# Optimization experiments

Measured on AMD Instinct MI355X. Metric: run time of the kernel, lower is better.

The kernel has to match this reference:

```python
import jax, jax.numpy as jnp
import numpy as np

B, P, ENC_DIM = 256, 196, 2048
WORD_DIM, ATT_DIM = 512, 512

def setup_inputs() -> dict:
    key = jax.random.key(0)
    ks = jax.random.split(key, 8)
    s_enc = 1.0 / np.sqrt(ENC_DIM)
    s_dec = 1.0 / np.sqrt(WORD_DIM)
    s_fin = 1.0 / np.sqrt(ATT_DIM)
    return {
        "encoder_out": jax.random.normal(ks[0], (B, P, ENC_DIM), dtype=jnp.float32),
        "decoder_out": jax.random.normal(ks[1], (B, WORD_DIM), dtype=jnp.float32),
        "W_enc": jax.random.uniform(ks[2], (ENC_DIM, ATT_DIM), jnp.float32, -s_enc, s_enc),
        "b_enc": jax.random.uniform(ks[3], (ATT_DIM,), jnp.float32, -s_enc, s_enc),
        "W_dec": jax.random.uniform(ks[4], (WORD_DIM, ATT_DIM), jnp.float32, -s_dec, s_dec),
        "b_dec": jax.random.uniform(ks[5], (ATT_DIM,), jnp.float32, -s_dec, s_dec),
        "W_fin": jax.random.uniform(ks[6], (ATT_DIM,), jnp.float32, -s_fin, s_fin),
        "b_fin": jax.random.uniform(ks[7], (), jnp.float32, -s_fin, s_fin),
    }

def reference(encoder_out, decoder_out, W_enc, b_enc, W_dec, b_dec, W_fin, b_fin):
    # encoder projection: [B, P, A]
    att_enc = jnp.einsum('bpe,ea->bpa', encoder_out, W_enc) + b_enc
    # decoder projection: [B, A]
    att_dec = decoder_out @ W_dec + b_dec
    # additive combine + relu + final scalar projection -> [B, P]
    hidden = jax.nn.relu(att_enc + att_dec[:, None, :])
    att = jnp.einsum('bpa,a->bp', hidden, W_fin) + b_fin
    # softmax over pixels (dim=1)
    att_weights = jax.nn.softmax(att, axis=1)
    # weighted sum of encoder features -> [B, ENC_DIM]
    return jnp.einsum('bpe,bp->be', encoder_out, att_weights)
```

## Files before the change

### kernel.cpp

```cpp
#include <hip/hip_runtime.h>

#define B_   256
#define P_   196
#define E_   2048
#define WD_  512
#define A_   512
#define M_   (B_ * P_)

typedef __bf16 bf16x8 __attribute__((ext_vector_type(8)));
typedef float  f32x4  __attribute__((ext_vector_type(4)));

using u16 = unsigned short;
using u32 = unsigned int;

__device__ inline u16 f2bf(float f) {
    u32 u; __builtin_memcpy(&u, &f, 4);
    u += 0x7FFFu + ((u >> 16) & 1u); return (u16)(u >> 16);
}

__global__ __launch_bounds__(256) void k_prep(const float* __restrict__ We,
                                              u16* __restrict__ Wt) {
    __shared__ float tile[32][33];
    const int tx = threadIdx.x & 31, ty = threadIdx.x >> 5;
    const int k0 = blockIdx.x * 32, n0 = blockIdx.y * 32;
#pragma unroll
    for (int i = 0; i < 4; ++i)
        tile[ty + i * 8][tx] = We[(size_t)(k0 + ty + i * 8) * A_ + n0 + tx];
    __syncthreads();
#pragma unroll
    for (int i = 0; i < 4; ++i)
        Wt[(size_t)(n0 + ty + i * 8) * E_ + k0 + tx] = f2bf(tile[tx][ty + i * 8]);
}

__global__ __launch_bounds__(512) void k_att_dec(const float* __restrict__ dec,
                                                 const float* __restrict__ Wd,
                                                 const float* __restrict__ bd,
                                                 float* __restrict__ att_dec) {
    int b = blockIdx.x, a = threadIdx.x;
    __shared__ float sd[WD_];
    sd[a] = dec[b * WD_ + a];
    __syncthreads();
    float acc = bd[a];
#pragma unroll 8
    for (int e = 0; e < WD_; ++e)
        acc = fmaf(sd[e], Wd[e * A_ + a], acc);
    att_dec[b * A_ + a] = acc;
}

__global__ __launch_bounds__(512, 2) void k_logits(
        const float* __restrict__ enc, const u16* __restrict__ Wt,
        const float* __restrict__ be, const float* __restrict__ Wf,
        const float* __restrict__ att_dec, float* __restrict__ att) {
    __shared__ bf16x8 sA[2][256];
    __shared__ float  sred[8][64];

    const int t   = threadIdx.x;
    const int w   = t >> 6;
    const int L   = t & 63;
    const int l15 = L & 15;
    const int q   = L >> 4;
    const int m0  = blockIdx.x * 64;

    const f32x4 zero = {0.f, 0.f, 0.f, 0.f};
    f32x4 acc[4][4];
#pragma unroll
    for (int rt = 0; rt < 4; ++rt)
#pragma unroll
        for (int ct = 0; ct < 4; ++ct) acc[rt][ct] = zero;

    const int s    = t >> 1, h = t & 1;
    const int srt  = s >> 6;
    const int sL   = s & 63;
    const float* ap = enc + (size_t)(m0 + srt * 16 + (sL & 15)) * E_
                          + (sL >> 4) * 8 + h * 4;
    u32* slds = (u32*)&sA[0][s] + h * 2;
    u32* slds1 = (u32*)&sA[1][s] + h * 2;

    const u16* bp = Wt + (size_t)(w * 64 + l15) * E_ + q * 8;
    const size_t bstep = (size_t)16 * E_;

    uint4 bcur[4], bnxt[4];
#pragma unroll
    for (int ct = 0; ct < 4; ++ct)
        bcur[ct] = *(const uint4*)(bp + ct * bstep);
    float4 aN1 = *(const float4*)(ap);
    float4 aN2 = *(const float4*)(ap + 32);
    {
        u32 lo = (u32)f2bf(aN1.x) | ((u32)f2bf(aN1.y) << 16);
        u32 hi = (u32)f2bf(aN1.z) | ((u32)f2bf(aN1.w) << 16);
        slds[0] = lo; slds[1] = hi;
    }
    aN1 = aN2;
    __syncthreads();

    for (int k = 0; k < 64; ++k) {
        const int buf = k & 1;
        bf16x8 af[4];
#pragma unroll
        for (int rt = 0; rt < 4; ++rt) af[rt] = sA[buf][rt * 64 + L];

        const int kA = (k + 2 < 64) ? k + 2 : 63;
        const int kB = (k + 1 < 64) ? k + 1 : 63;
        aN2 = *(const float4*)(ap + (size_t)kA * 32);
#pragma unroll
        for (int ct = 0; ct < 4; ++ct)
            bnxt[ct] = *(const uint4*)(bp + ct * bstep + (size_t)kB * 32);

#pragma unroll
        for (int ct = 0; ct < 4; ++ct) {
            bf16x8 bv; __builtin_memcpy(&bv, &bcur[ct], 16);
#pragma unroll
            for (int rt = 0; rt < 4; ++rt)
                acc[rt][ct] = __builtin_amdgcn_mfma_f32_16x16x32_bf16(
                    af[rt], bv, acc[rt][ct], 0, 0, 0);
        }

        {
            u32 lo = (u32)f2bf(aN1.x) | ((u32)f2bf(aN1.y) << 16);
            u32 hi = (u32)f2bf(aN1.z) | ((u32)f2bf(aN1.w) << 16);
            u32* d = buf ? slds : slds1;
            d[0] = lo; d[1] = hi;
        }
        aN1 = aN2;
#pragma unroll
        for (int ct = 0; ct < 4; ++ct) bcur[ct] = bnxt[ct];
        __syncthreads();
    }

    float wf[4], bev[4];
#pragma unroll
    for (int ct = 0; ct < 4; ++ct) {
        int n = w * 64 + ct * 16 + l15;
        wf[ct]  = Wf[n];
        bev[ct] = be[n];
    }
#pragma unroll
    for (int rt = 0; rt < 4; ++rt) {
#pragma unroll
        for (int reg = 0; reg < 4; ++reg) {
            int ml = rt * 16 + q * 4 + reg;
            int b  = (m0 + ml) / P_;
            const float* adp = att_dec + (size_t)b * A_ + w * 64 + l15;
            float p = 0.f;
#pragma unroll
            for (int ct = 0; ct < 4; ++ct) {
                float hx = acc[rt][ct][reg] + bev[ct] + adp[ct * 16];
                p = fmaf(fmaxf(hx, 0.f), wf[ct], p);
            }
#pragma unroll
            for (int off = 8; off > 0; off >>= 1)
                p += __shfl_down(p, off, 16);
            if (l15 == 0) sred[w][ml] = p;
        }
    }
    __syncthreads();
    if (t < 64) {
        float r = 0.f;
#pragma unroll
        for (int ww = 0; ww < 8; ++ww) r += sred[ww][t];
        att[m0 + t] = r;
    }
}

__global__ __launch_bounds__(256) void k_out(const float* __restrict__ enc,
                                             const float* __restrict__ att,
                                             float* __restrict__ out) {
    int b = blockIdx.x, t = threadIdx.x;
    __shared__ float sw[P_];
    __shared__ float red[8];
    __shared__ f32x4 spart[4][64];

    float v = (t < P_) ? att[b * P_ + t] : -1e30f;
    float m = v;
#pragma unroll
    for (int off = 32; off > 0; off >>= 1)
        m = fmaxf(m, __shfl_down(m, off, 64));
    int wid = t >> 6;
    if ((t & 63) == 0) red[wid] = m;
    __syncthreads();
    m = fmaxf(fmaxf(red[0], red[1]), fmaxf(red[2], red[3]));

    float ev = (t < P_) ? __expf(v - m) : 0.f;
    float ssum = ev;
#pragma unroll
    for (int off = 32; off > 0; off >>= 1)
        ssum += __shfl_down(ssum, off, 64);
    if ((t & 63) == 0) red[4 + wid] = ssum;
    __syncthreads();
    ssum = red[4] + red[5] + red[6] + red[7];
    if (t < P_) sw[t] = ev / ssum;
    __syncthreads();

    const int tq = t >> 6, lane = t & 63;
    const int e0 = blockIdx.y * 256 + lane * 4;
    const float* ep = enc + (size_t)b * P_ * E_ + e0;
    f32x4 acc = {0.f, 0.f, 0.f, 0.f};
    const int p0 = tq * 49;
#pragma unroll 7
    for (int i = 0; i < 49; ++i) {
        int p = p0 + i;
        float4 qv = *(const float4*)(ep + (size_t)p * E_);
        float wgt = sw[p];
        acc[0] = fmaf(wgt, qv.x, acc[0]);
        acc[1] = fmaf(wgt, qv.y, acc[1]);
        acc[2] = fmaf(wgt, qv.z, acc[2]);
        acc[3] = fmaf(wgt, qv.w, acc[3]);
    }
    spart[tq][lane] = acc;
    __syncthreads();
    if (tq == 0) {
        f32x4 r = spart[0][lane];
#pragma unroll
        for (int g = 1; g < 4; ++g) {
            f32x4 x = spart[g][lane];
            r[0] += x[0]; r[1] += x[1]; r[2] += x[2]; r[3] += x[3];
        }
        float* op = out + (size_t)b * E_ + e0;
        op[0] = r[0]; op[1] = r[1]; op[2] = r[2]; op[3] = r[3];
    }
}

extern "C" void kernel_launch(void* const* d_in, const int* in_sizes, int n_in,
                              void* d_out, int out_size, void* d_ws, size_t ws_size,
                              hipStream_t stream) {
    const float* enc   = (const float*)d_in[0];
    const float* dec   = (const float*)d_in[1];
    const float* W_enc = (const float*)d_in[2];
    const float* b_enc = (const float*)d_in[3];
    const float* W_dec = (const float*)d_in[4];
    const float* b_dec = (const float*)d_in[5];
    const float* W_fin = (const float*)d_in[6];

    float* att_dec = (float*)d_ws;
    float* att     = att_dec + B_ * A_;
    u16*   Wt      = (u16*)(att + M_);

    k_prep<<<dim3(E_ / 32, A_ / 32), 256, 0, stream>>>(W_enc, Wt);
    k_att_dec<<<B_, 512, 0, stream>>>(dec, W_dec, b_dec, att_dec);
    k_logits<<<M_ / 64, 512, 0, stream>>>(enc, Wt, b_enc, W_fin, att_dec, att);
    k_out<<<dim3(B_, 8), 256, 0, stream>>>(enc, att, (float*)d_out);
}
```

Baseline: 872.4 us.

## Stage W_enc tiles into swizzled LDS via async global_load_lds double buffer

The bf16 weight operand in the logits GEMM is now copied straight from global memory into a double-buffered LDS tile using `global_load_lds`, with an XOR-swizzled slot layout. The MFMA B fragments are then read from LDS instead of prefetched through registers. This is meant to cut the VGPRs held by the B prefetch and let the copy run asynchronously. The launch bound is raised to 4 blocks per CU. The roughly 74KB of LDS per block probably still caps residency at 2 blocks, so the tighter register budget could cause spills without any occupancy gain.

```diff
diff --git a/kernel.cpp b/kernel.cpp
--- a/kernel.cpp
+++ b/kernel.cpp
@@ -16,6 +16,12 @@
 __device__ inline u16 f2bf(float f) {
     u32 u; __builtin_memcpy(&u, &f, 4);
     u += 0x7FFFu + ((u >> 16) & 1u); return (u16)(u >> 16);
+}
+
+__device__ inline void gld_lds16(const void* g, void* l) {
+    __builtin_amdgcn_global_load_lds(
+        (const __attribute__((address_space(1))) u32*)g,
+        (__attribute__((address_space(3))) u32*)l, 16, 0, 0);
 }
 
 __global__ __launch_bounds__(256) void k_prep(const float* __restrict__ We,
@@ -47,10 +53,11 @@
     att_dec[b * A_ + a] = acc;
 }
 
-__global__ __launch_bounds__(512, 2) void k_logits(
+__global__ __launch_bounds__(512, 4) void k_logits(
         const float* __restrict__ enc, const u16* __restrict__ Wt,
         const float* __restrict__ be, const float* __restrict__ Wf,
         const float* __restrict__ att_dec, float* __restrict__ att) {
+    __shared__ u16    sB[2][A_ * 32];
     __shared__ bf16x8 sA[2][256];
     __shared__ float  sred[8][64];
 
@@ -73,16 +80,26 @@
     const int sL   = s & 63;
     const float* ap = enc + (size_t)(m0 + srt * 16 + (sL & 15)) * E_
                           + (sL >> 4) * 8 + h * 4;
-    u32* slds = (u32*)&sA[0][s] + h * 2;
+    u32* slds  = (u32*)&sA[0][s] + h * 2;
     u32* slds1 = (u32*)&sA[1][s] + h * 2;
 
-    const u16* bp = Wt + (size_t)(w * 64 + l15) * E_ + q * 8;
-    const size_t bstep = (size_t)16 * E_;
-
-    uint4 bcur[4], bnxt[4];
-#pragma unroll
-    for (int ct = 0; ct < 4; ++ct)
-        bcur[ct] = *(const uint4*)(bp + ct * bstep);
+    const int brow  = L >> 2;
+    const int bslot = (L & 3) ^ ((L >> 3) & 3);
+    const u16* bsrc = Wt + (size_t)(w * 64 + brow) * E_ + bslot * 8;
+    u16* bdst0 = &sB[0][(w * 64) * 32];
+    u16* bdst1 = &sB[1][(w * 64) * 32];
+
+    int bro[4];
+#pragma unroll
+    for (int ct = 0; ct < 4; ++ct) {
+        int n = w * 64 + ct * 16 + l15;
+        int slot = q ^ ((l15 >> 1) & 3);
+        bro[ct] = n * 32 + slot * 8;
+    }
+
+#pragma unroll
+    for (int j = 0; j < 4; ++j)
+        gld_lds16(bsrc + (size_t)j * 16 * E_, bdst0 + j * 512);
     float4 aN1 = *(const float4*)(ap);
     float4 aN2 = *(const float4*)(ap + 32);
     {
@@ -93,26 +110,34 @@
     aN1 = aN2;
     __syncthreads();
 
-    for (int k = 0; k < 64; ++k) {
-        const int buf = k & 1;
+    for (int kt = 0; kt < 64; ++kt) {
+        const int buf = kt & 1;
+
+        if (kt < 63) {
+            const u16* bs = bsrc + (size_t)(kt + 1) * 32;
+            u16* bd = buf ? bdst0 : bdst1;
+#pragma unroll
+            for (int j = 0; j < 4; ++j)
+                gld_lds16(bs + (size_t)j * 16 * E_, bd + j * 512);
+        }
+        const int kA = (kt + 2 < 64) ? kt + 2 : 63;
+        aN2 = *(const float4*)(ap + (size_t)kA * 32);
+
         bf16x8 af[4];
 #pragma unroll
         for (int rt = 0; rt < 4; ++rt) af[rt] = sA[buf][rt * 64 + L];
-
-        const int kA = (k + 2 < 64) ? k + 2 : 63;
-        const int kB = (k + 1 < 64) ? k + 1 : 63;
-        aN2 = *(const float4*)(ap + (size_t)kA * 32);
+        const u16* sbb = sB[buf];
+        bf16x8 bv[4];
 #pragma unroll
         for (int ct = 0; ct < 4; ++ct)
-            bnxt[ct] = *(const uint4*)(bp + ct * bstep + (size_t)kB * 32);
+            __builtin_memcpy(&bv[ct], sbb + bro[ct], 16);
 
 #pragma unroll
         for (int ct = 0; ct < 4; ++ct) {
-            bf16x8 bv; __builtin_memcpy(&bv, &bcur[ct], 16);
 #pragma unroll
             for (int rt = 0; rt < 4; ++rt)
                 acc[rt][ct] = __builtin_amdgcn_mfma_f32_16x16x32_bf16(
-                    af[rt], bv, acc[rt][ct], 0, 0, 0);
+                    af[rt], bv[ct], acc[rt][ct], 0, 0, 0);
         }
 
         {
@@ -122,8 +147,7 @@
             d[0] = lo; d[1] = hi;
         }
         aN1 = aN2;
-#pragma unroll
-        for (int ct = 0; ct < 4; ++ct) bcur[ct] = bnxt[ct];
+
         __syncthreads();
     }
 
```

Measured after the change: 804.4 us. 7.8% less time.
